# Kernel optimization log

Measured on AMD Instinct MI355X. Metric: run time of the kernel, lower is better.

## Reference

```python
import jax, jax.numpy as jnp
from jax import lax
import numpy as np

PATCH = 8
THRESHOLD = 0.2  # learned per-layer threshold, at init value


def conv2d(x, w, b, pad):
    # x: (N,C,H,W), w: (O,I,kh,kw)
    y = lax.conv_general_dilated(x, w, (1, 1), [(pad, pad), (pad, pad)],
                                 dimension_numbers=('NCHW', 'OIHW', 'NCHW'))
    return y + b[None, :, None, None]


def extract_patches(X, p):
    # Appends 4 positional channels, then splits into non-overlapping p x p patches.
    B, C, H, W = X.shape
    gy, gx = jnp.meshgrid(jnp.linspace(0.0, 1.0, H), jnp.linspace(0.0, 1.0, W), indexing='ij')
    pos = jnp.stack([gx, gy, jnp.sin(jnp.pi * gx), jnp.sin(jnp.pi * gy)]).astype(X.dtype)  # (4,H,W)
    Xc = jnp.concatenate([X, jnp.broadcast_to(pos[None], (B, 4, H, W))], axis=1)  # (B,C+4,H,W)
    h, w = H // p, W // p
    Xp = Xc.reshape(B, C + 4, h, p, w, p).transpose(0, 2, 4, 1, 3, 5).reshape(B, h * w, C + 4, p, p)
    return Xp, h, w


def _forward(X,
             proj_w0, proj_b0, exp_w0, exp_b0, fin_w0, fin_b0,
             proj_w1, proj_b1, exp_w1, exp_b1, fin_w1, fin_b1,
             proj_w2, proj_b2, exp_w2, exp_b2, fin_w2, fin_b2,
             proj_w3, proj_b3, exp_w3, exp_b3, fin_w3, fin_b3,
             router_w, router_b, lin_w, lin_b):
    layers = [
        (proj_w0, proj_b0, exp_w0, exp_b0, fin_w0, fin_b0),
        (proj_w1, proj_b1, exp_w1, exp_b1, fin_w1, fin_b1),
        (proj_w2, proj_b2, exp_w2, exp_b2, fin_w2, fin_b2),
        (proj_w3, proj_b3, exp_w3, exp_b3, fin_w3, fin_b3),
    ]
    for (pw, pb, ew, eb, fw, fb) in layers:
        Xp, h, w = extract_patches(X, PATCH)        # (B,P,C,p,p)
        B, P, C, pH, pW = Xp.shape
        flat = Xp.reshape(B * P, C, pH, pW)
        # router: conv-proj -> global avg pool -> linear -> softmax
        pooled = conv2d(flat, pw, pb, 1).mean(axis=(2, 3))                 # (BP, 8)
        scores = jax.nn.softmax(pooled @ router_w.T + router_b, axis=-1)  # (BP, E)
        scores = scores.reshape(B, P, -1)                                  # (B,P,E)
        # all experts as one grouped conv: (E,Co,C,3,3) -> (E*Co,C,3,3)
        E, Co = ew.shape[0], ew.shape[1]
        eo = conv2d(flat, ew.reshape(E * Co, C, 3, 3), eb.reshape(E * Co), 1)
        eo = jax.nn.relu(eo).reshape(B, P, E, Co, pH, pW)
        # expert is skipped unless some patch score exceeds the layer threshold
        gate = (scores.max(axis=(0, 1)) > THRESHOLD).astype(X.dtype)        # (E,)
        comb = jnp.einsum('bpechw,bpe->bpchw', eo, scores * gate[None, None, :])
        img = comb.reshape(B, h, w, Co, pH, pW).transpose(0, 3, 1, 4, 2, 5)
        img = img.reshape(B, Co, h * pH, w * pW)
        X = conv2d(img, fw, fb, 4)  # 1x1 conv, padding=4 -> H,W grow by 8
    return X.reshape(X.shape[0], -1) @ lin_w.T + lin_b


def setup_inputs() -> dict:
    key = jax.random.key(0)
    ks = iter(jax.random.split(key, 64))

    def nrm(shape, fan_in):
        return jax.random.normal(next(ks), shape, jnp.float32) / np.sqrt(fan_in)

    d = {"X": jax.random.normal(next(ks), (16, 3, 64, 64), jnp.float32)}
    cin = [7, 68, 68, 132]   # expert/key input channels per layer (prev out + 4 pos)
    cout = [64, 64, 128, 128]
    E = 4
    for l in range(4):
        d[f"proj_w{l}"] = nrm((8, cin[l], 3, 3), cin[l] * 9)
        d[f"proj_b{l}"] = jnp.zeros((8,), jnp.float32)
        d[f"exp_w{l}"] = nrm((E, cout[l], cin[l], 3, 3), cin[l] * 9)
        d[f"exp_b{l}"] = jnp.zeros((E, cout[l]), jnp.float32)
        d[f"fin_w{l}"] = nrm((cout[l], cout[l], 1, 1), cout[l])
        d[f"fin_b{l}"] = jnp.zeros((cout[l],), jnp.float32)
    d["router_w"] = nrm((E, 8), 8)
    d["router_b"] = jnp.zeros((E,), jnp.float32)
    feat = 128 * 96 * 96  # final (B,128,96,96) flattened
    d["lin_w"] = nrm((10, feat), feat)
    d["lin_b"] = jnp.zeros((10,), jnp.float32)
    return d


def reference(X,
              proj_w0, proj_b0, exp_w0, exp_b0, fin_w0, fin_b0,
              proj_w1, proj_b1, exp_w1, exp_b1, fin_w1, fin_b1,
              proj_w2, proj_b2, exp_w2, exp_b2, fin_w2, fin_b2,
              proj_w3, proj_b3, exp_w3, exp_b3, fin_w3, fin_b3,
              router_w, router_b, lin_w, lin_b):
    return _forward(X,
                    proj_w0, proj_b0, exp_w0, exp_b0, fin_w0, fin_b0,
                    proj_w1, proj_b1, exp_w1, exp_b1, fin_w1, fin_b1,
                    proj_w2, proj_b2, exp_w2, exp_b2, fin_w2, fin_b2,
                    proj_w3, proj_b3, exp_w3, exp_b3, fin_w3, fin_b3,
                    router_w, router_b, lin_w, lin_b)
```

## Files before the change

kernel.cpp:

```cpp
#include <hip/hip_runtime.h>
#include <math.h>

#define NB 16
#define NE 4
#define THRESH 0.2f
#define LIN_NS 64

typedef __attribute__((ext_vector_type(8))) _Float16 f16x8;
typedef __attribute__((ext_vector_type(4))) float f32x4;
typedef unsigned short u16;
typedef unsigned int u32;

__device__ inline u16 f16bits(float v) { _Float16 h = (_Float16)v; return __builtin_bit_cast(u16, h); }

__global__ void repack_all_kernel(const float* __restrict__ ew, const float* __restrict__ fw,
    u16* __restrict__ Wm, u16* __restrict__ Wp, u16* __restrict__ fW,
    int CO, int CIN, int CINp, int C) {
    const int M = NE * CO;
    const int n1 = 9 * M * CINp, n2 = M * 64, n3 = CO * CO;
    const int n = n1 + n2 + n3;
    for (int i = blockIdx.x * blockDim.x + threadIdx.x; i < n; i += gridDim.x * blockDim.x) {
        if (i < n1) {
            int k = i % CINp; int t = i / CINp; int m = t % M; int ij = t / M;
            float v = (k < CIN) ? ew[(m * C + k) * 9 + ij] : 0.f;
            Wm[i] = f16bits(v);
        } else if (i < n1 + n2) {
            int j = i - n1; int kp = j & 63; int m = j >> 6;
            float v = 0.f;
            if (kp < 36) { int pc = kp / 9, ij = kp % 9; v = ew[(m * C + CIN + pc) * 9 + ij]; }
            Wp[j] = f16bits(v);
        } else {
            int j = i - n1 - n2;
            fW[j] = f16bits(fw[j]);
        }
    }
}

template<int CIN, int C>
__global__ __launch_bounds__(256) void router_kernel(
    const float* __restrict__ X, const float* __restrict__ pw, const float* __restrict__ pb,
    const float* __restrict__ rw, const float* __restrict__ rb,
    float* __restrict__ scores, int H, int W, int nP)
{
    __shared__ float S[4][C * 9 + 8];
    const int wv = threadIdx.x >> 6;
    const int lane = threadIdx.x & 63;
    const int bp = blockIdx.x * 4 + wv;
    const int P = nP * nP;
    const int b = bp / P, pi = bp % P;
    const int py = pi / nP, px = pi % nP;
    const int h = lane >> 3, w = lane & 7;
    const int gy = py * 8 + h, gx = px * 8 + w;
    float* Sw = S[wv];
    for (int c = 0; c < C; ++c) {
        float v;
        if (c < CIN) {
            v = X[(((size_t)b * CIN + c) * H + gy) * W + gx];
        } else {
            float t = (c == CIN || c == CIN + 2) ? gx * (1.f / (W - 1)) : gy * (1.f / (H - 1));
            v = (c >= CIN + 2) ? sinf(3.14159265358979323846f * t) : t;
        }
        float r = v;
        r += __shfl_xor(r, 1); r += __shfl_xor(r, 2); r += __shfl_xor(r, 4);
        float cc = v;
        cc += __shfl_xor(cc, 8); cc += __shfl_xor(cc, 16); cc += __shfl_xor(cc, 32);
        float T = r;
        T += __shfl_xor(T, 8); T += __shfl_xor(T, 16); T += __shfl_xor(T, 32);
        float R0 = __shfl(r, 0), R7 = __shfl(r, 56);
        float C0 = __shfl(cc, 0), C7 = __shfl(cc, 7);
        float x00 = __shfl(v, 0), x07 = __shfl(v, 7);
        float x70 = __shfl(v, 56), x77 = __shfl(v, 63);
        if (lane < 9) {
            int i = lane / 3, j = lane % 3;
            float s = T;
            if (i == 0) s -= R7; else if (i == 2) s -= R0;
            if (j == 0) s -= C7; else if (j == 2) s -= C0;
            if (i == 0 && j == 0) s += x77;
            else if (i == 0 && j == 2) s += x70;
            else if (i == 2 && j == 0) s += x07;
            else if (i == 2 && j == 2) s += x00;
            Sw[c * 9 + lane] = s;
        }
    }
    __syncthreads();
    if (lane < 8) {
        const int o = lane;
        float acc = 0.f;
        for (int c = 0; c < C; ++c) {
            #pragma unroll
            for (int ij = 0; ij < 9; ++ij)
                acc += pw[(o * C + c) * 9 + ij] * Sw[c * 9 + ij];
        }
        Sw[C * 9 + o] = acc * (1.f / 64.f) + pb[o];
    }
    __syncthreads();
    if (lane == 0) {
        float lg[NE];
        float m = -1e30f;
        #pragma unroll
        for (int e = 0; e < NE; ++e) {
            float a = rb[e];
            #pragma unroll
            for (int o = 0; o < 8; ++o) a += Sw[C * 9 + o] * rw[e * 8 + o];
            lg[e] = a;
            m = fmaxf(m, a);
        }
        float ssum = 0.f;
        #pragma unroll
        for (int e = 0; e < NE; ++e) { lg[e] = __expf(lg[e] - m); ssum += lg[e]; }
        float inv = 1.f / ssum;
        #pragma unroll
        for (int e = 0; e < NE; ++e) scores[bp * NE + e] = lg[e] * inv;
    }
}

__global__ __launch_bounds__(256) void gate_kernel(const float* __restrict__ scores, int BP,
                                                   float* __restrict__ gate)
{
    __shared__ float sm[4][NE];
    float m[NE] = {-1e30f, -1e30f, -1e30f, -1e30f};
    for (int i = threadIdx.x; i < BP; i += 256) {
        #pragma unroll
        for (int e = 0; e < NE; ++e) m[e] = fmaxf(m[e], scores[i * NE + e]);
    }
    #pragma unroll
    for (int e = 0; e < NE; ++e) {
        float v = m[e];
        for (int o = 32; o; o >>= 1) v = fmaxf(v, __shfl_xor(v, o));
        m[e] = v;
    }
    int wv = threadIdx.x >> 6, lane = threadIdx.x & 63;
    if (lane == 0) {
        #pragma unroll
        for (int e = 0; e < NE; ++e) sm[wv][e] = m[e];
    }
    __syncthreads();
    if (threadIdx.x == 0) {
        #pragma unroll
        for (int e = 0; e < NE; ++e) {
            float mx = fmaxf(fmaxf(sm[0][e], sm[1][e]), fmaxf(sm[2][e], sm[3][e]));
            gate[e] = (mx > THRESH) ? 1.f : 0.f;
        }
    }
}

__global__ __launch_bounds__(256) void border_kernel(float* __restrict__ Xn,
                                                     const float* __restrict__ fb,
                                                     int CO, int H, int W)
{
    const int Hout = H + 8, Wout = W + 8;
    const int nb = 16 * H + 64;
    const long total = (long)NB * CO * nb;
    for (long i = (long)blockIdx.x * blockDim.x + threadIdx.x; i < total;
         i += (long)gridDim.x * blockDim.x) {
        int j = (int)(i % nb); long t = i / nb; int o = (int)(t % CO); int b = (int)(t / CO);
        int y, x;
        if (j < 4 * Wout)       { y = j / Wout;             x = j % Wout; }
        else if (j < 8 * Wout)  { int j2 = j - 4 * Wout; y = H + 4 + j2 / Wout; x = j2 % Wout; }
        else                    { int j3 = j - 8 * Wout; y = 4 + j3 / 8;
                                  int c8 = j3 % 8; x = (c8 < 4) ? c8 : W + 4 + (c8 - 4); }
        Xn[(((size_t)b * CO + o) * Hout + y) * Wout + x] = fb[o];
    }
}

template<int CIN, int CINp, int CO>
__global__ __launch_bounds__(512, 2) void expert_fused_kernel(
    const float* __restrict__ X,
    const u16* __restrict__ Wm, const u16* __restrict__ Wp, const u16* __restrict__ fW,
    const float* __restrict__ eb, const float* __restrict__ fb,
    const float* __restrict__ scores, const float* __restrict__ gate,
    float* __restrict__ Xn, int H, int W, int nP)
{
    constexpr int M = NE * CO;
    constexpr int KSM = CINp / 32;
    constexpr int LOGK = (KSM == 4) ? 2 : (KSM == 2 ? 1 : 0);
    constexpr int NS = 9 * KSM;
    constexpr int SP = CINp + 8;
    constexpr int PIP = 72;
    constexpr int CP = CO + 8;
    constexpr bool FAT = (CO == 128);
    constexpr int NT = FAT ? 8 : 4;
    constexpr int PATW = 2 * 100 * SP;
    constexpr int POSW = 2 * 64 * PIP;
    constexpr int COMBW = 2 * 64 * CP;
    constexpr int SMW = (PATW + POSW > COMBW) ? (PATW + POSW) : COMBW;

    __shared__ __align__(16) u16 smem[SMW];
    __shared__ float pospix[2][4][64];
    u16* pat = smem;
    u16* posim = smem + PATW;
    u16* comb = smem;

    const int P = nP * nP;
    const int bp0 = blockIdx.x * 2, bp1 = bp0 + 1;
    const int b0 = bp0 / P, pi0 = bp0 % P, py0 = pi0 / nP, px0 = pi0 % nP;
    const int b1 = bp1 / P, pi1 = bp1 % P, py1 = pi1 / nP, px1 = pi1 % nP;
    const int tid = threadIdx.x;
    const int Hout = H + 8, Wout = W + 8;

    for (int i = tid; i < 100 * SP; i += 512) ((u32*)pat)[i] = 0;
    {
        int g = tid >> 8, r = tid & 255, pc = r >> 6, p = r & 63;
        int gy = (g ? py1 : py0) * 8 + (p >> 3), gx = (g ? px1 : px0) * 8 + (p & 7);
        float t = (pc == 0 || pc == 2) ? gx * (1.f / (W - 1)) : gy * (1.f / (H - 1));
        pospix[g][pc][p] = (pc >= 2) ? sinf(3.14159265358979323846f * t) : t;
    }
    __syncthreads();
    for (int i = tid; i < 2 * CIN * 16; i += 512) {
        int g = i / (CIN * 16), j = i % (CIN * 16);
        int c = j >> 4, q = j & 15, h = q >> 1, w4 = (q & 1) * 4;
        int bb = g ? b1 : b0, py = g ? py1 : py0, px = g ? px1 : px0;
        const float4 v = *(const float4*)&X[(((size_t)bb * CIN + c) * H + py * 8 + h) * W + px * 8 + w4];
        int base = g * 100 * SP + c;
        pat[base + ((h + 1) * 10 + (w4 + 1)) * SP] = f16bits(v.x);
        pat[base + ((h + 1) * 10 + (w4 + 2)) * SP] = f16bits(v.y);
        pat[base + ((h + 1) * 10 + (w4 + 3)) * SP] = f16bits(v.z);
        pat[base + ((h + 1) * 10 + (w4 + 4)) * SP] = f16bits(v.w);
    }
    for (int i = tid; i < 2 * 64 * 64; i += 512) {
        int g = i >> 12, r = i & 4095, pix = r >> 6, kp = r & 63;
        float v = 0.f;
        if (kp < 36) {
            int pc = kp / 9, ij = kp % 9;
            int hh = (pix >> 3) + ij / 3 - 1, ww = (pix & 7) + ij % 3 - 1;
            if (hh >= 0 && hh < 8 && ww >= 0 && ww < 8) v = pospix[g][pc][hh * 8 + ww];
        }
        posim[g * 64 * PIP + pix * PIP + kp] = f16bits(v);
    }
    __syncthreads();

    const int lane = tid & 63, wv = tid >> 6;
    const int colp = lane & 15, kg = lane >> 4;
    const int cot = FAT ? wv : (wv & 3);
    const int gO = FAT ? 0 : (wv >> 2);
    const int co0 = cot * 16;

    int prow[NT];
    #pragma unroll
    for (int nt = 0; nt < NT; ++nt) {
        int g = FAT ? (nt >> 2) : gO;
        int pix = (nt & 3) * 16 + colp;
        prow[nt] = g * 100 * SP + ((pix >> 3) * 10 + (pix & 7)) * SP;
    }
    int aoff[NE];
    #pragma unroll
    for (int e = 0; e < NE; ++e)
        aoff[e] = (e * CO + co0 + colp) * CINp + kg * 8;

    f32x4 acc[NE][NT];
    #pragma unroll
    for (int e = 0; e < NE; ++e)
        #pragma unroll
        for (int nt = 0; nt < NT; ++nt) acc[e][nt] = (f32x4){0.f, 0.f, 0.f, 0.f};

    f16x8 A0[NE], A1[NE];
    auto ldA = [&](int s, f16x8* A) {
        int ij = s >> LOGK, ks = s & (KSM - 1);
        const u16* Ws = Wm + (size_t)(ij * M) * CINp + ks * 32;
        #pragma unroll
        for (int e = 0; e < NE; ++e) A[e] = *(const f16x8*)(Ws + aoff[e]);
    };
    auto doStep = [&](int s, f16x8* A) {
        int ij = s >> LOGK, ks = s & (KSM - 1);
        int i3 = ij / 3;
        int tb = (i3 * 10 + (ij - 3 * i3)) * SP + ks * 32 + kg * 8;
        #pragma unroll
        for (int nt = 0; nt < NT; ++nt) {
            f16x8 Bv = *(const f16x8*)&pat[prow[nt] + tb];
            __builtin_amdgcn_s_setprio(1);
            #pragma unroll
            for (int e = 0; e < NE; ++e)
                acc[e][nt] = __builtin_amdgcn_mfma_f32_16x16x32_f16(A[e], Bv, acc[e][nt], 0, 0, 0);
            __builtin_amdgcn_s_setprio(0);
        }
    };

    ldA(0, A0);
    int s = 0;
    for (; s + 1 < NS; s += 2) {
        ldA(s + 1, A1);
        doStep(s, A0);
        ldA((s + 2 < NS) ? s + 2 : s + 1, A0);
        doStep(s + 1, A1);
    }
    if (s < NS) doStep(s, A0);

    #pragma unroll
    for (int ks = 0; ks < 2; ++ks) {
        #pragma unroll
        for (int e = 0; e < NE; ++e) {
            int ao = (e * CO + co0 + colp) * 64 + ks * 32 + kg * 8;
            A0[e] = *(const f16x8*)(Wp + ao);
        }
        #pragma unroll
        for (int nt = 0; nt < NT; ++nt) {
            int g = FAT ? (nt >> 2) : gO;
            int pix = (nt & 3) * 16 + colp;
            f16x8 Bv = *(const f16x8*)&posim[g * 64 * PIP + pix * PIP + ks * 32 + kg * 8];
            __builtin_amdgcn_s_setprio(1);
            #pragma unroll
            for (int e = 0; e < NE; ++e)
                acc[e][nt] = __builtin_amdgcn_mfma_f32_16x16x32_f16(A0[e], Bv, acc[e][nt], 0, 0, 0);
            __builtin_amdgcn_s_setprio(0);
        }
    }

    float sg0[NE], sg1[NE];
    #pragma unroll
    for (int e = 0; e < NE; ++e) {
        float gv = gate[e];
        sg0[e] = scores[bp0 * NE + e] * gv;
        sg1[e] = scores[bp1 * NE + e] * gv;
    }
    float ebv[NE][4];
    #pragma unroll
    for (int e = 0; e < NE; ++e)
        #pragma unroll
        for (int r = 0; r < 4; ++r) ebv[e][r] = eb[e * CO + co0 + kg * 4 + r];

    __syncthreads();

    #pragma unroll
    for (int nt = 0; nt < NT; ++nt) {
        const int g = FAT ? (nt >> 2) : gO;
        int pix = (nt & 3) * 16 + colp;
        u16 hv[4];
        #pragma unroll
        for (int r = 0; r < 4; ++r) {
            float cv = 0.f;
            #pragma unroll
            for (int e = 0; e < NE; ++e) {
                float s2 = g ? sg1[e] : sg0[e];
                cv += s2 * fmaxf(acc[e][nt][r] + ebv[e][r], 0.f);
            }
            hv[r] = f16bits(cv);
        }
        uint2 q;
        q.x = (u32)hv[0] | ((u32)hv[1] << 16);
        q.y = (u32)hv[2] | ((u32)hv[3] << 16);
        *(uint2*)&comb[g * 64 * CP + pix * CP + co0 + kg * 4] = q;
    }
    __syncthreads();

    const int o0 = co0;
    f32x4 accF[NT];
    #pragma unroll
    for (int nt = 0; nt < NT; ++nt) accF[nt] = (f32x4){0.f, 0.f, 0.f, 0.f};
    #pragma unroll
    for (int ks = 0; ks < CO / 32; ++ks) {
        int ao = (o0 + colp) * CO + ks * 32 + kg * 8;
        f16x8 ah = *(const f16x8*)(fW + ao);
        __builtin_amdgcn_s_setprio(1);
        #pragma unroll
        for (int nt = 0; nt < NT; ++nt) {
            int g = FAT ? (nt >> 2) : gO;
            int pix = (nt & 3) * 16 + colp;
            f16x8 bv = *(const f16x8*)&comb[g * 64 * CP + pix * CP + ks * 32 + kg * 8];
            accF[nt] = __builtin_amdgcn_mfma_f32_16x16x32_f16(ah, bv, accF[nt], 0, 0, 0);
        }
        __builtin_amdgcn_s_setprio(0);
    }
    float fbv[4];
    #pragma unroll
    for (int r = 0; r < 4; ++r) fbv[r] = fb[o0 + kg * 4 + r];
    #pragma unroll
    for (int nt = 0; nt < NT; ++nt) {
        const int g = FAT ? (nt >> 2) : gO;
        int pix = (nt & 3) * 16 + colp;
        int bb = g ? b1 : b0, py = g ? py1 : py0, px = g ? px1 : px0;
        int gy = py * 8 + (pix >> 3) + 4, gx = px * 8 + (pix & 7) + 4;
        #pragma unroll
        for (int r = 0; r < 4; ++r) {
            int o = o0 + kg * 4 + r;
            Xn[(((size_t)bb * CO + o) * Hout + gy) * Wout + gx] = accF[nt][r] + fbv[r];
        }
    }
}

__global__ __launch_bounds__(256) void linear_part_kernel(
    const float* __restrict__ Xf, const float* __restrict__ lw, float* __restrict__ part)
{
    const int feat = 128 * 96 * 96;
    const int CH = feat / LIN_NS;
    const int b = blockIdx.x / LIN_NS, s = blockIdx.x % LIN_NS;
    const float4* xa = (const float4*)(Xf + (size_t)b * feat + (size_t)s * CH);
    const float* wbase = lw + (size_t)s * CH;
    float acc[10];
    #pragma unroll
    for (int o = 0; o < 10; ++o) acc[o] = 0.f;
    const int n4 = CH / 4;
    for (int i = threadIdx.x; i < n4; i += 256) {
        float4 xv = xa[i];
        #pragma unroll
        for (int o = 0; o < 10; ++o) {
            float4 wv = *(const float4*)(wbase + (size_t)o * feat + i * 4);
            acc[o] += xv.x * wv.x + xv.y * wv.y + xv.z * wv.z + xv.w * wv.w;
        }
    }
    #pragma unroll
    for (int o = 0; o < 10; ++o)
        for (int m = 32; m; m >>= 1) acc[o] += __shfl_xor(acc[o], m);
    __shared__ float sm[4][10];
    int wv = threadIdx.x >> 6, lane = threadIdx.x & 63;
    if (lane == 0) {
        #pragma unroll
        for (int o = 0; o < 10; ++o) sm[wv][o] = acc[o];
    }
    __syncthreads();
    if (threadIdx.x < 10)
        part[(b * LIN_NS + s) * 10 + threadIdx.x] =
            sm[0][threadIdx.x] + sm[1][threadIdx.x] + sm[2][threadIdx.x] + sm[3][threadIdx.x];
}

__global__ __launch_bounds__(256) void linear_reduce_kernel(
    const float* __restrict__ part, const float* __restrict__ lb, float* __restrict__ out)
{
    int i = threadIdx.x;
    if (i < 160) {
        int b = i / 10, o = i % 10;
        float a = lb[o];
        for (int s = 0; s < LIN_NS; ++s) a += part[(b * LIN_NS + s) * 10 + o];
        out[i] = a;
    }
}

template<int CIN, int CINp, int CO>
static void run_layer(const float* Xin, int H, int nP, const float* const* Lw,
                      const float* rw, const float* rb,
                      const u16* Wm, const u16* Wp, const u16* fW,
                      float* scores, float* gate, float* Xn, hipStream_t stream)
{
    const int W = H;
    const int BP = NB * nP * nP;
    const float* pw = Lw[0]; const float* pb = Lw[1];
    const float* ebias = Lw[3];
    const float* fb = Lw[5];

    router_kernel<CIN, CIN + 4><<<BP / 4, 256, 0, stream>>>(Xin, pw, pb, rw, rb, scores, H, W, nP);
    gate_kernel<<<1, 256, 0, stream>>>(scores, BP, gate);
    border_kernel<<<2048, 256, 0, stream>>>(Xn, fb, CO, H, W);
    expert_fused_kernel<CIN, CINp, CO><<<BP / 2, 512, 0, stream>>>(
        Xin, Wm, Wp, fW, ebias, fb, scores, gate, Xn, H, W, nP);
}

extern "C" void kernel_launch(void* const* d_in, const int* in_sizes, int n_in,
                              void* d_out, int out_size, void* d_ws, size_t ws_size,
                              hipStream_t stream)
{
    const float* X0 = (const float*)d_in[0];
    const float* L[4][6];
    for (int l = 0; l < 4; ++l)
        for (int k = 0; k < 6; ++k) L[l][k] = (const float*)d_in[1 + l * 6 + k];
    const float* rw = (const float*)d_in[25];
    const float* rb = (const float*)d_in[26];
    const float* lw = (const float*)d_in[27];
    const float* lb = (const float*)d_in[28];

    char* ws = (char*)d_ws;
    const size_t XA_B = 63438848;
    const size_t XB_B = 75497472;
    float* XA = (float*)(ws);
    float* XB = (float*)(ws + XA_B);
    char* wp = ws + XA_B + XB_B;
    const int cfg_CO[4]   = {64, 64, 128, 128};
    const int cfg_CINp[4] = {32, 64, 64, 128};
    u16 *Wm[4], *Wp[4], *fW[4];
    for (int l = 0; l < 4; ++l) {
        int M = NE * cfg_CO[l];
        Wm[l] = (u16*)wp;            wp += (size_t)9 * M * cfg_CINp[l] * 2;
        Wp[l] = (u16*)wp;            wp += (size_t)M * 64 * 2;
        fW[l] = (u16*)wp;            wp += (size_t)cfg_CO[l] * cfg_CO[l] * 2;
    }
    float* scores = (float*)wp;
    float* gate = scores + 1936 * 4;
    float* lpart = gate + 16;

    const int cfg_CIN[4] = {3, 64, 64, 128};
    for (int l = 0; l < 4; ++l)
        repack_all_kernel<<<512, 256, 0, stream>>>(L[l][2], L[l][4], Wm[l], Wp[l], fW[l],
                                                   cfg_CO[l], cfg_CIN[l], cfg_CINp[l], cfg_CIN[l] + 4);

    run_layer<3,   32,  64>(X0, 64,  8, L[0], rw, rb, Wm[0], Wp[0], fW[0], scores, gate, XA, stream);
    run_layer<64,  64,  64>(XA, 72,  9, L[1], rw, rb, Wm[1], Wp[1], fW[1], scores, gate, XB, stream);
    run_layer<64,  64, 128>(XB, 80, 10, L[2], rw, rb, Wm[2], Wp[2], fW[2], scores, gate, XA, stream);
    run_layer<128, 128, 128>(XA, 88, 11, L[3], rw, rb, Wm[3], Wp[3], fW[3], scores, gate, XB, stream);

    linear_part_kernel<<<16 * LIN_NS, 256, 0, stream>>>(XB, lw, lpart);
    linear_reduce_kernel<<<1, 256, 0, stream>>>(lpart, lb, (float*)d_out);
}
```

Before: 789.8 us.

## Fuse gate into expert kernel, fold layer-0 input into posim, batch linear

Drops the separate gate kernel. Each expert block now recomputes the global per-expert max of the scores itself and applies the threshold. For the 3-channel first layer, the input channels are folded into the positional im2col tile and weight block, so the main MFMA loop and the patch zeroing are skipped. The final linear kernel now processes four batch items per block, so each weight chunk is loaded once per four images instead of once per image. In exchange every expert block redundantly rescans all scores, and the gate step adds more shared memory and a reduction.

After: 787.7 us, median of 2. No clear change (-0.3%).

```diff
diff --git a/kernel.cpp b/kernel.cpp
--- a/kernel.cpp
+++ b/kernel.cpp
@@ -27,7 +27,12 @@
         } else if (i < n1 + n2) {
             int j = i - n1; int kp = j & 63; int m = j >> 6;
             float v = 0.f;
-            if (kp < 36) { int pc = kp / 9, ij = kp % 9; v = ew[(m * C + CIN + pc) * 9 + ij]; }
+            if (CIN == 3) {
+                if (kp < 27)      { int c = kp / 9,  ij = kp % 9;  v = ew[(m * C + c) * 9 + ij]; }
+                else if (kp < 63) { int q = kp - 27; int pc = q / 9, ij = q % 9; v = ew[(m * C + 3 + pc) * 9 + ij]; }
+            } else {
+                if (kp < 36) { int pc = kp / 9, ij = kp % 9; v = ew[(m * C + CIN + pc) * 9 + ij]; }
+            }
             Wp[j] = f16bits(v);
         } else {
             int j = i - n1 - n2;
@@ -114,36 +119,6 @@
     }
 }
 
-__global__ __launch_bounds__(256) void gate_kernel(const float* __restrict__ scores, int BP,
-                                                   float* __restrict__ gate)
-{
-    __shared__ float sm[4][NE];
-    float m[NE] = {-1e30f, -1e30f, -1e30f, -1e30f};
-    for (int i = threadIdx.x; i < BP; i += 256) {
-        #pragma unroll
-        for (int e = 0; e < NE; ++e) m[e] = fmaxf(m[e], scores[i * NE + e]);
-    }
-    #pragma unroll
-    for (int e = 0; e < NE; ++e) {
-        float v = m[e];
-        for (int o = 32; o; o >>= 1) v = fmaxf(v, __shfl_xor(v, o));
-        m[e] = v;
-    }
-    int wv = threadIdx.x >> 6, lane = threadIdx.x & 63;
-    if (lane == 0) {
-        #pragma unroll
-        for (int e = 0; e < NE; ++e) sm[wv][e] = m[e];
-    }
-    __syncthreads();
-    if (threadIdx.x == 0) {
-        #pragma unroll
-        for (int e = 0; e < NE; ++e) {
-            float mx = fmaxf(fmaxf(sm[0][e], sm[1][e]), fmaxf(sm[2][e], sm[3][e]));
-            gate[e] = (mx > THRESH) ? 1.f : 0.f;
-        }
-    }
-}
-
 __global__ __launch_bounds__(256) void border_kernel(float* __restrict__ Xn,
                                                      const float* __restrict__ fb,
                                                      int CO, int H, int W)
@@ -168,7 +143,7 @@
     const float* __restrict__ X,
     const u16* __restrict__ Wm, const u16* __restrict__ Wp, const u16* __restrict__ fW,
     const float* __restrict__ eb, const float* __restrict__ fb,
-    const float* __restrict__ scores, const float* __restrict__ gate,
+    const float* __restrict__ scores, int BPtot,
     float* __restrict__ Xn, int H, int W, int nP)
 {
     constexpr int M = NE * CO;
@@ -179,6 +154,7 @@
     constexpr int PIP = 72;
     constexpr int CP = CO + 8;
     constexpr bool FAT = (CO == 128);
+    constexpr bool UNI = (CIN == 3);
     constexpr int NT = FAT ? 8 : 4;
     constexpr int PATW = 2 * 100 * SP;
     constexpr int POSW = 2 * 64 * PIP;
@@ -187,6 +163,8 @@
 
     __shared__ __align__(16) u16 smem[SMW];
     __shared__ float pospix[2][4][64];
+    __shared__ float xpix[2][3][64];
+    __shared__ float gsh[8][NE];
     u16* pat = smem;
     u16* posim = smem + PATW;
     u16* comb = smem;
@@ -198,34 +176,77 @@
     const int tid = threadIdx.x;
     const int Hout = H + 8, Wout = W + 8;
 
-    for (int i = tid; i < 100 * SP; i += 512) ((u32*)pat)[i] = 0;
+    if constexpr (!UNI) {
+        for (int i = tid; i < 100 * SP; i += 512) ((u32*)pat)[i] = 0;
+    }
     {
         int g = tid >> 8, r = tid & 255, pc = r >> 6, p = r & 63;
         int gy = (g ? py1 : py0) * 8 + (p >> 3), gx = (g ? px1 : px0) * 8 + (p & 7);
         float t = (pc == 0 || pc == 2) ? gx * (1.f / (W - 1)) : gy * (1.f / (H - 1));
         pospix[g][pc][p] = (pc >= 2) ? sinf(3.14159265358979323846f * t) : t;
     }
-    __syncthreads();
-    for (int i = tid; i < 2 * CIN * 16; i += 512) {
-        int g = i / (CIN * 16), j = i % (CIN * 16);
-        int c = j >> 4, q = j & 15, h = q >> 1, w4 = (q & 1) * 4;
-        int bb = g ? b1 : b0, py = g ? py1 : py0, px = g ? px1 : px0;
-        const float4 v = *(const float4*)&X[(((size_t)bb * CIN + c) * H + py * 8 + h) * W + px * 8 + w4];
-        int base = g * 100 * SP + c;
-        pat[base + ((h + 1) * 10 + (w4 + 1)) * SP] = f16bits(v.x);
-        pat[base + ((h + 1) * 10 + (w4 + 2)) * SP] = f16bits(v.y);
-        pat[base + ((h + 1) * 10 + (w4 + 3)) * SP] = f16bits(v.z);
-        pat[base + ((h + 1) * 10 + (w4 + 4)) * SP] = f16bits(v.w);
+    if constexpr (UNI) {
+        for (int i = tid; i < 2 * 3 * 64; i += 512) {
+            int g = i / 192, r = i % 192, c = r >> 6, p = r & 63;
+            int bb = g ? b1 : b0, py = g ? py1 : py0, px = g ? px1 : px0;
+            xpix[g][c][p] = X[(((size_t)bb * CIN + c) * H + py * 8 + (p >> 3)) * W + px * 8 + (p & 7)];
+        }
+    }
+    float gm[NE] = {-1e30f, -1e30f, -1e30f, -1e30f};
+    for (int i = tid; i < BPtot; i += 512) {
+        float4 sc = ((const float4*)scores)[i];
+        gm[0] = fmaxf(gm[0], sc.x); gm[1] = fmaxf(gm[1], sc.y);
+        gm[2] = fmaxf(gm[2], sc.z); gm[3] = fmaxf(gm[3], sc.w);
+    }
+    __syncthreads();
+
+    if constexpr (!UNI) {
+        for (int i = tid; i < 2 * CIN * 16; i += 512) {
+            int g = i / (CIN * 16), j = i % (CIN * 16);
+            int c = j >> 4, q = j & 15, h = q >> 1, w4 = (q & 1) * 4;
+            int bb = g ? b1 : b0, py = g ? py1 : py0, px = g ? px1 : px0;
+            const float4 v = *(const float4*)&X[(((size_t)bb * CIN + c) * H + py * 8 + h) * W + px * 8 + w4];
+            int base = g * 100 * SP + c;
+            pat[base + ((h + 1) * 10 + (w4 + 1)) * SP] = f16bits(v.x);
+            pat[base + ((h + 1) * 10 + (w4 + 2)) * SP] = f16bits(v.y);
+            pat[base + ((h + 1) * 10 + (w4 + 3)) * SP] = f16bits(v.z);
+            pat[base + ((h + 1) * 10 + (w4 + 4)) * SP] = f16bits(v.w);
+        }
     }
     for (int i = tid; i < 2 * 64 * 64; i += 512) {
         int g = i >> 12, r = i & 4095, pix = r >> 6, kp = r & 63;
         float v = 0.f;
-        if (kp < 36) {
-            int pc = kp / 9, ij = kp % 9;
-            int hh = (pix >> 3) + ij / 3 - 1, ww = (pix & 7) + ij % 3 - 1;
-            if (hh >= 0 && hh < 8 && ww >= 0 && ww < 8) v = pospix[g][pc][hh * 8 + ww];
+        if constexpr (UNI) {
+            if (kp < 27) {
+                int c = kp / 9, ij = kp % 9;
+                int hh = (pix >> 3) + ij / 3 - 1, ww = (pix & 7) + ij % 3 - 1;
+                if (hh >= 0 && hh < 8 && ww >= 0 && ww < 8) v = xpix[g][c][hh * 8 + ww];
+            } else if (kp < 63) {
+                int q = kp - 27; int pc = q / 9, ij = q % 9;
+                int hh = (pix >> 3) + ij / 3 - 1, ww = (pix & 7) + ij % 3 - 1;
+                if (hh >= 0 && hh < 8 && ww >= 0 && ww < 8) v = pospix[g][pc][hh * 8 + ww];
+            }
+        } else {
+            if (kp < 36) {
+                int pc = kp / 9, ij = kp % 9;
+                int hh = (pix >> 3) + ij / 3 - 1, ww = (pix & 7) + ij % 3 - 1;
+                if (hh >= 0 && hh < 8 && ww >= 0 && ww < 8) v = pospix[g][pc][hh * 8 + ww];
+            }
         }
         posim[g * 64 * PIP + pix * PIP + kp] = f16bits(v);
+    }
+    {
+        const int lane = tid & 63, wvi = tid >> 6;
+        #pragma unroll
+        for (int e = 0; e < NE; ++e) {
+            float v = gm[e];
+            for (int o = 32; o; o >>= 1) v = fmaxf(v, __shfl_xor(v, o));
+            gm[e] = v;
+        }
+        if (lane == 0) {
+            #pragma unroll
+            for (int e = 0; e < NE; ++e) gsh[wvi][e] = gm[e];
+        }
     }
     __syncthreads();
 
@@ -254,36 +275,37 @@
         for (int nt = 0; nt < NT; ++nt) acc[e][nt] = (f32x4){0.f, 0.f, 0.f, 0.f};
 
     f16x8 A0[NE], A1[NE];
-    auto ldA = [&](int s, f16x8* A) {
-        int ij = s >> LOGK, ks = s & (KSM - 1);
-        const u16* Ws = Wm + (size_t)(ij * M) * CINp + ks * 32;
-        #pragma unroll
-        for (int e = 0; e < NE; ++e) A[e] = *(const f16x8*)(Ws + aoff[e]);
-    };
-    auto doStep = [&](int s, f16x8* A) {
-        int ij = s >> LOGK, ks = s & (KSM - 1);
-        int i3 = ij / 3;
-        int tb = (i3 * 10 + (ij - 3 * i3)) * SP + ks * 32 + kg * 8;
-        #pragma unroll
-        for (int nt = 0; nt < NT; ++nt) {
-            f16x8 Bv = *(const f16x8*)&pat[prow[nt] + tb];
-            __builtin_amdgcn_s_setprio(1);
-            #pragma unroll
-            for (int e = 0; e < NE; ++e)
-                acc[e][nt] = __builtin_amdgcn_mfma_f32_16x16x32_f16(A[e], Bv, acc[e][nt], 0, 0, 0);
-            __builtin_amdgcn_s_setprio(0);
-        }
-    };
-
-    ldA(0, A0);
-    int s = 0;
-    for (; s + 1 < NS; s += 2) {
-        ldA(s + 1, A1);
-        doStep(s, A0);
-        ldA((s + 2 < NS) ? s + 2 : s + 1, A0);
-        doStep(s + 1, A1);
-    }
-    if (s < NS) doStep(s, A0);
+    if constexpr (!UNI) {
+        auto ldA = [&](int s, f16x8* A) {
+            int ij = s >> LOGK, ks = s & (KSM - 1);
+            const u16* Ws = Wm + (size_t)(ij * M) * CINp + ks * 32;
+            #pragma unroll
+            for (int e = 0; e < NE; ++e) A[e] = *(const f16x8*)(Ws + aoff[e]);
+        };
+        auto doStep = [&](int s, f16x8* A) {
+            int ij = s >> LOGK, ks = s & (KSM - 1);
+            int i3 = ij / 3;
+            int tb = (i3 * 10 + (ij - 3 * i3)) * SP + ks * 32 + kg * 8;
+            #pragma unroll
+            for (int nt = 0; nt < NT; ++nt) {
+                f16x8 Bv = *(const f16x8*)&pat[prow[nt] + tb];
+                __builtin_amdgcn_s_setprio(1);
+                #pragma unroll
+                for (int e = 0; e < NE; ++e)
+                    acc[e][nt] = __builtin_amdgcn_mfma_f32_16x16x32_f16(A[e], Bv, acc[e][nt], 0, 0, 0);
+                __builtin_amdgcn_s_setprio(0);
+            }
+        };
+        ldA(0, A0);
+        int s = 0;
+        for (; s + 1 < NS; s += 2) {
+            ldA(s + 1, A1);
+            doStep(s, A0);
+            ldA((s + 2 < NS) ? s + 2 : s + 1, A0);
+            doStep(s + 1, A1);
+        }
+        if (s < NS) doStep(s, A0);
+    }
 
     #pragma unroll
     for (int ks = 0; ks < 2; ++ks) {
@@ -308,7 +330,10 @@
     float sg0[NE], sg1[NE];
     #pragma unroll
     for (int e = 0; e < NE; ++e) {
-        float gv = gate[e];
+        float mx = gsh[0][e];
+        #pragma unroll
+        for (int w8 = 1; w8 < 8; ++w8) mx = fmaxf(mx, gsh[w8][e]);
+        float gv = (mx > THRESH) ? 1.f : 0.f;
         sg0[e] = scores[bp0 * NE + e] * gv;
         sg1[e] = scores[bp1 * NE + e] * gv;
     }
@@ -382,34 +407,48 @@
 {
     const int feat = 128 * 96 * 96;
     const int CH = feat / LIN_NS;
-    const int b = blockIdx.x / LIN_NS, s = blockIdx.x % LIN_NS;
-    const float4* xa = (const float4*)(Xf + (size_t)b * feat + (size_t)s * CH);
-    const float* wbase = lw + (size_t)s * CH;
-    float acc[10];
-    #pragma unroll
-    for (int o = 0; o < 10; ++o) acc[o] = 0.f;
+    const int s = blockIdx.x & (LIN_NS - 1);
+    const int bg = blockIdx.x / LIN_NS;
+    float acc[4][10];
+    #pragma unroll
+    for (int bb = 0; bb < 4; ++bb)
+        #pragma unroll
+        for (int o = 0; o < 10; ++o) acc[bb][o] = 0.f;
     const int n4 = CH / 4;
     for (int i = threadIdx.x; i < n4; i += 256) {
-        float4 xv = xa[i];
-        #pragma unroll
-        for (int o = 0; o < 10; ++o) {
-            float4 wv = *(const float4*)(wbase + (size_t)o * feat + i * 4);
-            acc[o] += xv.x * wv.x + xv.y * wv.y + xv.z * wv.z + xv.w * wv.w;
-        }
-    }
-    #pragma unroll
-    for (int o = 0; o < 10; ++o)
-        for (int m = 32; m; m >>= 1) acc[o] += __shfl_xor(acc[o], m);
-    __shared__ float sm[4][10];
-    int wv = threadIdx.x >> 6, lane = threadIdx.x & 63;
+        float4 wv[10];
+        #pragma unroll
+        for (int o = 0; o < 10; ++o)
+            wv[o] = *(const float4*)(lw + (size_t)o * feat + (size_t)s * CH + i * 4);
+        #pragma unroll
+        for (int bb = 0; bb < 4; ++bb) {
+            float4 xv = *(const float4*)(Xf + (size_t)(bg * 4 + bb) * feat + (size_t)s * CH + i * 4);
+            #pragma unroll
+            for (int o = 0; o < 10; ++o)
+                acc[bb][o] += xv.x * wv[o].x + xv.y * wv[o].y + xv.z * wv[o].z + xv.w * wv[o].w;
+        }
+    }
+    #pragma unroll
+    for (int bb = 0; bb < 4; ++bb)
+        #pragma unroll
+        for (int o = 0; o < 10; ++o)
+            for (int m = 32; m; m >>= 1) acc[bb][o] += __shfl_xor(acc[bb][o], m);
+    __shared__ float sm[4][40];
+    int wvi = threadIdx.x >> 6, lane = threadIdx.x & 63;
     if (lane == 0) {
         #pragma unroll
-        for (int o = 0; o < 10; ++o) sm[wv][o] = acc[o];
-    }
-    __syncthreads();
-    if (threadIdx.x < 10)
-        part[(b * LIN_NS + s) * 10 + threadIdx.x] =
-            sm[0][threadIdx.x] + sm[1][threadIdx.x] + sm[2][threadIdx.x] + sm[3][threadIdx.x];
+        for (int bb = 0; bb < 4; ++bb)
+            #pragma unroll
+            for (int o = 0; o < 10; ++o) sm[wvi][bb * 10 + o] = acc[bb][o];
+    }
+    __syncthreads();
+    int t = threadIdx.x;
+    if (t < 40) {
+        float a = sm[0][t] + sm[1][t] + sm[2][t] + sm[3][t];
+        int bb = t / 10, o = t % 10;
+        int b = bg * 4 + bb;
+        part[(b * LIN_NS + s) * 10 + o] = a;
+    }
 }
 
 __global__ __launch_bounds__(256) void linear_reduce_kernel(
@@ -428,7 +467,7 @@
 static void run_layer(const float* Xin, int H, int nP, const float* const* Lw,
                       const float* rw, const float* rb,
                       const u16* Wm, const u16* Wp, const u16* fW,
-                      float* scores, float* gate, float* Xn, hipStream_t stream)
+                      float* scores, float* Xn, hipStream_t stream)
 {
     const int W = H;
     const int BP = NB * nP * nP;
@@ -437,10 +476,9 @@
     const float* fb = Lw[5];
 
     router_kernel<CIN, CIN + 4><<<BP / 4, 256, 0, stream>>>(Xin, pw, pb, rw, rb, scores, H, W, nP);
-    gate_kernel<<<1, 256, 0, stream>>>(scores, BP, gate);
     border_kernel<<<2048, 256, 0, stream>>>(Xn, fb, CO, H, W);
     expert_fused_kernel<CIN, CINp, CO><<<BP / 2, 512, 0, stream>>>(
-        Xin, Wm, Wp, fW, ebias, fb, scores, gate, Xn, H, W, nP);
+        Xin, Wm, Wp, fW, ebias, fb, scores, BP, Xn, H, W, nP);
 }
 
 extern "C" void kernel_launch(void* const* d_in, const int* in_sizes, int n_in,
@@ -472,19 +510,18 @@
         fW[l] = (u16*)wp;            wp += (size_t)cfg_CO[l] * cfg_CO[l] * 2;
     }
     float* scores = (float*)wp;
-    float* gate = scores + 1936 * 4;
-    float* lpart = gate + 16;
+    float* lpart = scores + 1936 * 4;
 
     const int cfg_CIN[4] = {3, 64, 64, 128};
     for (int l = 0; l < 4; ++l)
         repack_all_kernel<<<512, 256, 0, stream>>>(L[l][2], L[l][4], Wm[l], Wp[l], fW[l],
                                                    cfg_CO[l], cfg_CIN[l], cfg_CINp[l], cfg_CIN[l] + 4);
 
-    run_layer<3,   32,  64>(X0, 64,  8, L[0], rw, rb, Wm[0], Wp[0], fW[0], scores, gate, XA, stream);
-    run_layer<64,  64,  64>(XA, 72,  9, L[1], rw, rb, Wm[1], Wp[1], fW[1], scores, gate, XB, stream);
-    run_layer<64,  64, 128>(XB, 80, 10, L[2], rw, rb, Wm[2], Wp[2], fW[2], scores, gate, XA, stream);
-    run_layer<128, 128, 128>(XA, 88, 11, L[3], rw, rb, Wm[3], Wp[3], fW[3], scores, gate, XB, stream);
-
-    linear_part_kernel<<<16 * LIN_NS, 256, 0, stream>>>(XB, lw, lpart);
+    run_layer<3,   32,  64>(X0, 64,  8, L[0], rw, rb, Wm[0], Wp[0], fW[0], scores, XA, stream);
+    run_layer<64,  64,  64>(XA, 72,  9, L[1], rw, rb, Wm[1], Wp[1], fW[1], scores, XB, stream);
+    run_layer<64,  64, 128>(XB, 80, 10, L[2], rw, rb, Wm[2], Wp[2], fW[2], scores, XA, stream);
+    run_layer<128, 128, 128>(XA, 88, 11, L[3], rw, rb, Wm[3], Wp[3], fW[3], scores, XB, stream);
+
+    linear_part_kernel<<<LIN_NS * (NB / 4), 256, 0, stream>>>(XB, lw, lpart);
     linear_reduce_kernel<<<1, 256, 0, stream>>>(lpart, lb, (float*)d_out);
 }
```
